# Optimization experiments

Hardware: AMD Instinct MI355X
Metric: run time of the kernel (lower is better)

The kernel has to match this reference:

```python
import jax, jax.numpy as jnp
import numpy as np

N, E, G, H, C, DIN, DE = 20000, 320000, 32, 8, 56, 32, 5
HC = H * C  # 448
NEG_SLOPE = 0.2
EPS_BN = 1e-5


def _seg_softmax(scores, seg, num):
    # scores: [E, H], softmax over edges sharing the same target node
    m = jax.ops.segment_max(scores, seg, num_segments=num)
    e = jnp.exp(scores - m[seg])
    s = jax.ops.segment_sum(e, seg, num_segments=num)
    return e / (s[seg] + 1e-16)


def _add_self_loops(src, dst, eattr, n):
    # PyG fill_value='mean': self-loop edge_attr = mean of incoming edge_attr
    deg = jax.ops.segment_sum(jnp.ones((src.shape[0],), eattr.dtype), dst, num_segments=n)
    esum = jax.ops.segment_sum(eattr, dst, num_segments=n)
    loop_attr = esum / jnp.maximum(deg, 1.0)[:, None]
    ar = jnp.arange(n, dtype=src.dtype)
    return (jnp.concatenate([src, ar]), jnp.concatenate([dst, ar]),
            jnp.concatenate([eattr, loop_attr], axis=0))


def _gatv2(x, src, dst, eattr, Wl, Wr, We, att, bias, n):
    xl = (x @ Wl).reshape(n, H, C)  # source transform (messages)
    xr = (x @ Wr).reshape(n, H, C)  # target transform
    ee = (eattr @ We).reshape(-1, H, C)
    s = jax.nn.leaky_relu(xl[src] + xr[dst] + ee, NEG_SLOPE)  # [E, H, C]
    score = jnp.einsum('ehc,hc->eh', s, att)
    alpha = _seg_softmax(score, dst, n)
    out = jax.ops.segment_sum(alpha[..., None] * xl[src], dst, num_segments=n)
    return out.reshape(n, HC) + bias


def _bn(x, gamma, beta):
    m = x.mean(axis=0)
    v = x.var(axis=0)  # biased variance, as torch BatchNorm1d (training)
    return (x - m) * jax.lax.rsqrt(v + EPS_BN) * gamma + beta


def setup_inputs() -> dict:
    key = jax.random.key(0)
    ks = jax.random.split(key, 18)
    sc = lambda k, shape: (jax.random.normal(k, shape, jnp.float32) * 0.05)
    return {
        'x': jax.random.normal(ks[0], (N, DIN), jnp.float32),
        'edge_index': jax.random.randint(ks[1], (2, E), 0, N),
        'edge_attr': jax.random.normal(ks[2], (E, DE), jnp.float32),
        'batch': jnp.sort(jax.random.randint(ks[3], (N,), 0, G)),
        'Wl1': sc(ks[4], (DIN, HC)), 'Wr1': sc(ks[5], (DIN, HC)),
        'We1': sc(ks[6], (DE, HC)), 'att1': sc(ks[7], (H, C)),
        'bias1': jnp.zeros((HC,), jnp.float32),
        'Wl2': sc(ks[8], (HC, HC)), 'Wr2': sc(ks[9], (HC, HC)),
        'We2': sc(ks[10], (DE, HC)), 'att2': sc(ks[11], (H, C)),
        'bias2': jnp.zeros((HC,), jnp.float32),
        'bn_gamma': jnp.ones((HC,), jnp.float32),
        'bn_beta': jnp.zeros((HC,), jnp.float32),
        'Wlin': sc(ks[12], (HC, 18)),
        'blin': jnp.zeros((18,), jnp.float32),
    }


def reference(x, edge_index, edge_attr, batch, Wl1, Wr1, We1, att1, bias1,
              Wl2, Wr2, We2, att2, bias2, bn_gamma, bn_beta, Wlin, blin):
    src, dst = edge_index[0], edge_index[1]
    src2, dst2, ea2 = _add_self_loops(src, dst, edge_attr, N)
    # dropout is identity in eval
    h = _gatv2(x, src2, dst2, ea2, Wl1, Wr1, We1, att1, bias1, N)
    h = jax.nn.elu(h)
    h = _bn(h, bn_gamma, bn_beta)
    h = _gatv2(h, src2, dst2, ea2, Wl2, Wr2, We2, att2, bias2, N)
    # global mean pool per graph
    cnt = jax.ops.segment_sum(jnp.ones((N,), h.dtype), batch, num_segments=G)
    pooled = jax.ops.segment_sum(h, batch, num_segments=G) / jnp.maximum(cnt, 1.0)[:, None]
    pooled = _bn(pooled, bn_gamma, bn_beta)
    logits = pooled @ Wlin + blin
    return jax.nn.log_softmax(logits, axis=1)
```

## Files before the change

kernel.cpp:

```cpp
#include <hip/hip_runtime.h>
#include <hip/hip_bf16.h>

#define NN   20000
#define EE   320000
#define EN   340000
#define HH   8
#define CC   56
#define HC   448
#define DEA  5
#define EAS  8
#define DINN 32
#define GG   32
#define NEG  0.2f

#define SS   896
#define MT   157
#define NT   7

typedef short bf16x8 __attribute__((ext_vector_type(8)));
typedef float f32x4  __attribute__((ext_vector_type(4)));
typedef float f32x8  __attribute__((ext_vector_type(8)));

static __device__ __forceinline__ unsigned short f2bf(float f) {
  unsigned int u = __float_as_uint(f);
  u += 0x7fffu + ((u >> 16) & 1u);
  return (unsigned short)(u >> 16);
}

static __device__ __forceinline__ f32x8 bf8_to_f32x8(uint4 u) {
  f32x8 o;
  o[0] = __uint_as_float(u.x << 16); o[1] = __uint_as_float(u.x & 0xffff0000u);
  o[2] = __uint_as_float(u.y << 16); o[3] = __uint_as_float(u.y & 0xffff0000u);
  o[4] = __uint_as_float(u.z << 16); o[5] = __uint_as_float(u.z & 0xffff0000u);
  o[6] = __uint_as_float(u.w << 16); o[7] = __uint_as_float(u.w & 0xffff0000u);
  return o;
}

static __device__ __forceinline__ float dpp8_sum(float x) {
  int v = __float_as_int(x);
  x += __int_as_float(__builtin_amdgcn_update_dpp(0, v, 0xB1, 0xF, 0xF, true));
  v = __float_as_int(x);
  x += __int_as_float(__builtin_amdgcn_update_dpp(0, v, 0x4E, 0xF, 0xF, true));
  v = __float_as_int(x);
  x += __int_as_float(__builtin_amdgcn_update_dpp(0, v, 0x141, 0xF, 0xF, true));
  return x;
}

__global__ void k_deg(const int* __restrict__ dst, int* deg) {
  int e = blockIdx.x * 256 + threadIdx.x;
  if (e < EE) atomicAdd(&deg[dst[e]], 1);
}

__global__ __launch_bounds__(1024) void k_scan(const int* __restrict__ deg, int* offs,
                                               int* cursor) {
  __shared__ int tot[1024];
  int t = threadIdx.x;
  int base = t * 20;
  int loc[20];
  int s = 0;
  #pragma unroll
  for (int i = 0; i < 20; i++) {
    int idx = base + i;
    int v = (idx < NN) ? deg[idx] + 1 : 0;
    loc[i] = s;
    s += v;
  }
  tot[t] = s;
  __syncthreads();
  for (int o = 1; o < 1024; o <<= 1) {
    int v = (t >= o) ? tot[t - o] : 0;
    __syncthreads();
    tot[t] += v;
    __syncthreads();
  }
  int basesum = (t == 0) ? 0 : tot[t - 1];
  #pragma unroll
  for (int i = 0; i < 20; i++) {
    int idx = base + i;
    if (idx < NN) { offs[idx] = basesum + loc[i]; cursor[idx] = basesum + loc[i]; }
  }
  if (t == 1023) offs[NN] = tot[1023];
}

#define XCN (NN * DINN)
#define W1N (SS * DINN)
#define W2N (SS * HC)
__global__ void k_scatter(const int* __restrict__ src, const int* __restrict__ dst,
                          const float* __restrict__ ea,
                          int* cursor, int* __restrict__ csr_src, float* __restrict__ csr_ea,
                          const float* __restrict__ x, unsigned short* __restrict__ xb,
                          const float* __restrict__ Wl1, const float* __restrict__ Wr1,
                          unsigned short* __restrict__ W1t,
                          const float* __restrict__ Wl2, const float* __restrict__ Wr2,
                          unsigned short* __restrict__ W2t) {
  int i = blockIdx.x * 256 + threadIdx.x;
  if (i < EE) {
    int d = dst[i], s = src[i];
    float a[DEA];
    #pragma unroll
    for (int j = 0; j < DEA; j++) a[j] = ea[(size_t)i * DEA + j];
    int pos = atomicAdd(&cursor[d], 1);
    csr_src[pos] = s;
    float* o = csr_ea + (size_t)pos * EAS;
    *(f32x4*)o       = (f32x4){a[0], a[1], a[2], a[3]};
    *(f32x4*)(o + 4) = (f32x4){a[4], 0.f, 0.f, 0.f};
    return;
  }
  i -= EE;
  if (i < XCN) { xb[i] = f2bf(x[i]); return; }
  i -= XCN;
  if (i < W1N) {
    int col = i / DINN, k = i - col * DINN;
    int cc = (col < HC) ? col : col - HC;
    const float* W = (col < HC) ? Wl1 : Wr1;
    W1t[i] = f2bf(W[(size_t)k * HC + cc]);
    return;
  }
  i -= W1N;
  if (i < W2N) {
    int col = i / HC, k = i - col * HC;
    int cc = (col < HC) ? col : col - HC;
    const float* W = (col < HC) ? Wl2 : Wr2;
    W2t[i] = f2bf(W[(size_t)k * HC + cc]);
  }
}

__global__ void k_aux(const int* __restrict__ offs,
                      int* __restrict__ csr_src, float* __restrict__ csr_ea) {
  int n = blockIdx.x * 256 + threadIdx.x;
  if (n >= NN) return;
  int e0 = offs[n], e1 = offs[n + 1] - 1;
  float a0 = 0.f, a1 = 0.f, a2 = 0.f, a3 = 0.f, a4 = 0.f;
  for (int e = e0; e < e1; e++) {
    const float* p = csr_ea + (size_t)e * EAS;
    a0 += p[0]; a1 += p[1]; a2 += p[2]; a3 += p[3]; a4 += p[4];
  }
  float inv = 1.f / fmaxf((float)(e1 - e0), 1.f);
  csr_src[e1] = n;
  float* o = csr_ea + (size_t)e1 * EAS;
  *(f32x4*)o       = (f32x4){a0 * inv, a1 * inv, a2 * inv, a3 * inv};
  *(f32x4*)(o + 4) = (f32x4){a4 * inv, 0.f, 0.f, 0.f};
}

__global__ __launch_bounds__(256) void k_gemm1(const unsigned short* __restrict__ xb,
                                               const unsigned short* __restrict__ W1t,
                                               unsigned short* __restrict__ out) {
  int w = threadIdx.x >> 6, lane = threadIdx.x & 63;
  int q = lane >> 4, r = lane & 15;
  int m0 = blockIdx.x * 64;
  int node = blockIdx.y * 64 + w * 16 + r;
  int nc = node < NN ? node : NN - 1;
  bf16x8 b = *(const bf16x8*)(xb + (size_t)nc * DINN + q * 8);
  #pragma unroll
  for (int j = 0; j < 4; j++) {
    bf16x8 a = *(const bf16x8*)(W1t + (size_t)(m0 + j * 16 + r) * DINN + q * 8);
    f32x4 acc = {0.f, 0.f, 0.f, 0.f};
    acc = __builtin_amdgcn_mfma_f32_16x16x32_bf16(a, b, acc, 0, 0, 0);
    uint2 st;
    st.x = ((unsigned int)f2bf(acc[1]) << 16) | f2bf(acc[0]);
    st.y = ((unsigned int)f2bf(acc[3]) << 16) | f2bf(acc[2]);
    if (node < NN)
      *(uint2*)(out + (size_t)node * SS + m0 + j * 16 + q * 4) = st;
  }
}

__global__ __launch_bounds__(256) void k_attn(
    const unsigned short* __restrict__ xlr,
    const int* __restrict__ offs, const int* __restrict__ csr_src,
    const float* __restrict__ csr_ea,
    const float* __restrict__ We, const float* __restrict__ att,
    const float* __restrict__ bias,
    unsigned short* __restrict__ outb, int layer1) {
  int n = __builtin_amdgcn_readfirstlane(blockIdx.x * 4 + (threadIdx.x >> 6));
  if (n >= NN) return;
  int lane = threadIdx.x & 63;
  int head = lane >> 3, sub = lane & 7;
  bool v = sub < 7;
  int cb = head * 56 + (v ? sub : 6) * 8;

  f32x8 z = {0.f,0.f,0.f,0.f,0.f,0.f,0.f,0.f};
  f32x8 xr = bf8_to_f32x8(*(const uint4*)(xlr + (size_t)n * SS + HC + cb));
  f32x8 at = *(const f32x8*)(att + cb);
  if (!v) at = z;
  f32x8 w0 = *(const f32x8*)(We + 0 * HC + cb);
  f32x8 w1 = *(const f32x8*)(We + 1 * HC + cb);
  f32x8 w2 = *(const f32x8*)(We + 2 * HC + cb);
  f32x8 w3 = *(const f32x8*)(We + 3 * HC + cb);
  f32x8 w4 = *(const f32x8*)(We + 4 * HC + cb);

  int e0 = offs[n], e1 = offs[n + 1];
  int last = e1 - 1;
  float l = 0.f;
  f32x8 acc = z;

  int sA[4];
  #pragma unroll
  for (int k = 0; k < 4; k++) {
    int ek = e0 + k; ek = ek < last ? ek : last;
    sA[k] = csr_src[__builtin_amdgcn_readfirstlane(ek)];
  }

  for (int e = e0; e < e1; e += 4) {
    uint4 g[4];
    #pragma unroll
    for (int k = 0; k < 4; k++)
      g[k] = *(const uint4*)(xlr + (size_t)sA[k] * SS + cb);
    int en = e + 4;
    if (en < e1) {
      #pragma unroll
      for (int k = 0; k < 4; k++) {
        int ek = en + k; ek = ek < last ? ek : last;
        sA[k] = csr_src[__builtin_amdgcn_readfirstlane(ek)];
      }
    }
    f32x8 md[4];
    #pragma unroll
    for (int k = 0; k < 4; k++) {
      int ek = e + k; ek = ek < last ? ek : last;
      md[k] = *(const f32x8*)(csr_ea + (size_t)__builtin_amdgcn_readfirstlane(ek) * EAS);
    }

    #pragma unroll
    for (int k = 0; k < 4; k++) {
      f32x8 tb = xr;
      tb += md[k][0] * w0; tb += md[k][1] * w1; tb += md[k][2] * w2;
      tb += md[k][3] * w3; tb += md[k][4] * w4;
      f32x8 xl = bf8_to_f32x8(g[k]);
      f32x8 t = tb + xl;
      #pragma unroll
      for (int i = 0; i < 8; i++) t[i] = fmaxf(t[i], NEG * t[i]);
      float p = 0.f;
      #pragma unroll
      for (int i = 0; i < 8; i++) p += t[i] * at[i];
      p = dpp8_sum(p);
      float wv = (e + k < e1) ? __expf(fminf(p, 60.f)) : 0.f;
      acc += wv * xl;
      l += wv;
    }
  }

  f32x8 b8 = *(const f32x8*)(bias + cb);
  f32x8 o = acc * (1.f / (l + 1e-16f)) + b8;
  if (v) {
    if (layer1) {
      #pragma unroll
      for (int i = 0; i < 8; i++) o[i] = o[i] > 0.f ? o[i] : (__expf(o[i]) - 1.f);
    }
    uint4 pk;
    pk.x = ((unsigned int)f2bf(o[1]) << 16) | f2bf(o[0]);
    pk.y = ((unsigned int)f2bf(o[3]) << 16) | f2bf(o[2]);
    pk.z = ((unsigned int)f2bf(o[5]) << 16) | f2bf(o[4]);
    pk.w = ((unsigned int)f2bf(o[7]) << 16) | f2bf(o[6]);
    *(uint4*)(outb + (size_t)n * HC + cb) = pk;
  }
}

__global__ __launch_bounds__(448) void k_bnstats(const unsigned short* __restrict__ h,
                                                 float* stat) {
  int c = threadIdx.x;
  int rows_per = (NN + gridDim.x - 1) / gridDim.x;
  int r0 = blockIdx.x * rows_per, r1 = min(NN, r0 + rows_per);
  float s = 0.f, sq = 0.f;
  for (int r = r0; r < r1; r++) {
    unsigned int u = h[(size_t)r * HC + c];
    float v = __uint_as_float(u << 16);
    s += v; sq += v * v;
  }
  atomicAdd(&stat[c], s);
  atomicAdd(&stat[HC + c], sq);
}

__global__ __launch_bounds__(64) void k_w2fix(const unsigned short* __restrict__ W2t,
                                              const float* __restrict__ stat,
                                              const float* __restrict__ gam,
                                              const float* __restrict__ bet,
                                              unsigned short* __restrict__ W2s,
                                              float* __restrict__ bias2) {
  int j = blockIdx.x;
  int t = threadIdx.x;
  float bacc = 0.f;
  #pragma unroll
  for (int it = 0; it < 7; it++) {
    int k = t + it * 64;
    float w = __uint_as_float((unsigned int)W2t[(size_t)j * HC + k] << 16);
    float mean = stat[k] * (1.f / NN);
    float var  = stat[HC + k] * (1.f / NN) - mean * mean;
    float sc = rsqrtf(var + 1e-5f) * gam[k];
    float sh = bet[k] - mean * sc;
    bacc += sh * w;
    W2s[(size_t)j * HC + k] = f2bf(sc * w);
  }
  #pragma unroll
  for (int m = 32; m >= 1; m >>= 1) bacc += __shfl_xor(bacc, m, 64);
  if (t == 0) bias2[j] = bacc;
}

__global__ __launch_bounds__(256) void k_gemm2(const unsigned short* __restrict__ A,
                                               const unsigned short* __restrict__ Bt,
                                               const float* __restrict__ bias2,
                                               unsigned short* __restrict__ out) {
  __shared__ unsigned short As[2 * 128 * 64];
  __shared__ unsigned short Bs[2 * 128 * 64];
  int bid = blockIdx.x;
  int g = bid / 56, rem = bid - g * 56;
  int xs = min(8, MT - g * 8);
  int bx = g * 8 + rem % xs;
  int by = rem / xs;
  int t = threadIdx.x;
  int w = t >> 6, lane = t & 63;
  int wm = w >> 1, wn = w & 1;
  int q = lane >> 4, r = lane & 15;
  int m0 = bx * 128;
  int n0 = by * 128;

  const unsigned short *ag[4], *bg[4];
  unsigned short *la[4], *lb[4];
  #pragma unroll
  for (int j = 0; j < 4; j++) {
    int s = t + j * 256;
    int row = s >> 3;
    int gcol = (s & 7) ^ (row & 7);
    int ar = m0 + row; if (ar >= NN) ar = NN - 1;
    ag[j] = A + (size_t)ar * HC + gcol * 8;
    bg[j] = Bt + (size_t)(n0 + row) * HC + gcol * 8;
    la[j] = As + s * 8;
    lb[j] = Bs + s * 8;
  }

  f32x4 zero = {0.f, 0.f, 0.f, 0.f};
  f32x4 acc[4][4];
  #pragma unroll
  for (int i = 0; i < 4; i++)
    #pragma unroll
    for (int j = 0; j < 4; j++) acc[i][j] = zero;

#define G2_STAGE(buf, k0)                                                     \
  _Pragma("unroll")                                                           \
  for (int j = 0; j < 4; j++) {                                               \
    __builtin_amdgcn_global_load_lds(                                         \
        (const __attribute__((address_space(1))) unsigned int*)(ag[j] + (k0)),\
        (__attribute__((address_space(3))) unsigned int*)(la[j] + (buf) * (128 * 64)), \
        16, 0, 0);                                                            \
    __builtin_amdgcn_global_load_lds(                                         \
        (const __attribute__((address_space(1))) unsigned int*)(bg[j] + (k0)),\
        (__attribute__((address_space(3))) unsigned int*)(lb[j] + (buf) * (128 * 64)), \
        16, 0, 0);                                                            \
  }

  G2_STAGE(0, 0);
  for (int st = 0; st < NT; ++st) {
    int cur = st & 1;
    if (st < NT - 1) {
      G2_STAGE(cur ^ 1, (st + 1) * 64);
      asm volatile("s_waitcnt vmcnt(8)" ::: "memory");
    } else {
      asm volatile("s_waitcnt vmcnt(0)" ::: "memory");
    }
    __builtin_amdgcn_s_barrier();
    const unsigned short* Asc = As + cur * (128 * 64);
    const unsigned short* Bsc = Bs + cur * (128 * 64);
    #pragma unroll
    for (int kk = 0; kk < 64; kk += 32) {
      int p = (kk >> 3) + q;
      bf16x8 af[4], bf[4];
      #pragma unroll
      for (int i = 0; i < 4; i++) {
        int row = wm * 64 + i * 16 + r;
        af[i] = *(const bf16x8*)(Asc + row * 64 + ((p ^ (r & 7)) * 8));
      }
      #pragma unroll
      for (int j = 0; j < 4; j++) {
        int row = wn * 64 + j * 16 + r;
        bf[j] = *(const bf16x8*)(Bsc + row * 64 + ((p ^ (r & 7)) * 8));
      }
      #pragma unroll
      for (int i = 0; i < 4; i++)
        #pragma unroll
        for (int j = 0; j < 4; j++)
          acc[i][j] = __builtin_amdgcn_mfma_f32_16x16x32_bf16(af[i], bf[j], acc[i][j], 0, 0, 0);
    }
    __builtin_amdgcn_s_barrier();
  }
#undef G2_STAGE

  #pragma unroll
  for (int j = 0; j < 4; j++) {
    int col = n0 + wn * 64 + j * 16 + r;
    float bs = bias2[col];
    #pragma unroll
    for (int i = 0; i < 4; i++) {
      int row_base = m0 + wm * 64 + i * 16 + q * 4;
      #pragma unroll
      for (int reg = 0; reg < 4; reg++) {
        int row = row_base + reg;
        if (row < NN) out[(size_t)row * SS + col] = f2bf(acc[i][j][reg] + bs);
      }
    }
  }
}

__global__ __launch_bounds__(448) void k_pool(const unsigned short* __restrict__ h2,
                                              const int* __restrict__ batch,
                                              float* pooled, int* cnt) {
  int c = threadIdx.x;
  int rows_per = (NN + gridDim.x - 1) / gridDim.x;
  int r0 = blockIdx.x * rows_per, r1 = min(NN, r0 + rows_per);
  if (r0 >= r1) return;
  float loc = 0.f;
  int rc = 0;
  int gcur = batch[r0];
  for (int r = r0; r < r1; r++) {
    int g = batch[r];
    if (g != gcur) {
      atomicAdd(&pooled[gcur * HC + c], loc);
      if (c == 0) atomicAdd(&cnt[gcur], rc);
      loc = 0.f; rc = 0; gcur = g;
    }
    unsigned int u = h2[(size_t)r * HC + c];
    loc += __uint_as_float(u << 16);
    rc++;
  }
  atomicAdd(&pooled[gcur * HC + c], loc);
  if (c == 0) atomicAdd(&cnt[gcur], rc);
}

__global__ __launch_bounds__(448) void k_final(const float* __restrict__ pooled_sum,
                                               const int* __restrict__ cnt,
                                               const float* __restrict__ gam,
                                               const float* __restrict__ bet,
                                               const float* __restrict__ Wlin,
                                               const float* __restrict__ blin,
                                               float* __restrict__ out) {
  __shared__ float P[GG * HC];
  __shared__ float L[GG * 18];
  __shared__ float red[GG];
  int c = threadIdx.x;
  float s = 0.f, sq = 0.f;
  for (int g = 0; g < GG; g++) {
    float v = pooled_sum[g * HC + c] / fmaxf((float)cnt[g], 1.f);
    P[g * HC + c] = v; s += v; sq += v * v;
  }
  float mean = s * (1.f / GG);
  float var  = sq * (1.f / GG) - mean * mean;
  float sc = rsqrtf(var + 1e-5f) * gam[c];
  float sh = bet[c] - mean * sc;
  for (int g = 0; g < GG; g++) P[g * HC + c] = P[g * HC + c] * sc + sh;
  __syncthreads();
  for (int o = c; o < GG * 18; o += HC) {
    int g = o / 18, j = o - g * 18;
    float acc = blin[j];
    for (int k = 0; k < HC; k++) acc += P[g * HC + k] * Wlin[k * 18 + j];
    L[o] = acc;
  }
  __syncthreads();
  if (c < GG) {
    float mx = -3.4e38f;
    for (int j = 0; j < 18; j++) mx = fmaxf(mx, L[c * 18 + j]);
    float se = 0.f;
    for (int j = 0; j < 18; j++) se += __expf(L[c * 18 + j] - mx);
    red[c] = mx + logf(se);
  }
  __syncthreads();
  for (int o = c; o < GG * 18; o += HC) out[o] = L[o] - red[o / 18];
}

extern "C" void kernel_launch(void* const* d_in, const int* in_sizes, int n_in,
                              void* d_out, int out_size, void* d_ws, size_t ws_size,
                              hipStream_t stream) {
  (void)in_sizes; (void)n_in; (void)out_size; (void)ws_size;
  const float* x     = (const float*)d_in[0];
  const int*   ei    = (const int*)d_in[1];
  const float* ea    = (const float*)d_in[2];
  const int*   batch = (const int*)d_in[3];
  const float* Wl1   = (const float*)d_in[4];
  const float* Wr1   = (const float*)d_in[5];
  const float* We1   = (const float*)d_in[6];
  const float* att1  = (const float*)d_in[7];
  const float* bias1 = (const float*)d_in[8];
  const float* Wl2   = (const float*)d_in[9];
  const float* Wr2   = (const float*)d_in[10];
  const float* We2   = (const float*)d_in[11];
  const float* att2  = (const float*)d_in[12];
  const float* bias2in = (const float*)d_in[13];
  const float* gam   = (const float*)d_in[14];
  const float* bet   = (const float*)d_in[15];
  const float* Wlin  = (const float*)d_in[16];
  const float* blin  = (const float*)d_in[17];
  float* out = (float*)d_out;
  const int* srcp = ei;
  const int* dstp = ei + EE;

  char* ws = (char*)d_ws;
  size_t off = 0;
  auto alloc = [&](size_t bytes) -> char* {
    char* p = ws + off;
    off = (off + bytes + 255) & ~(size_t)255;
    return p;
  };
  int*   deg     = (int*)  alloc(NN * 4);
  float* bnstat  = (float*)alloc(HC * 2 * 4);
  float* pooled  = (float*)alloc(GG * HC * 4 + GG * 4);
  int*   cnt     = (int*)(pooled + GG * HC);
  size_t zlen    = (size_t)((char*)(cnt + GG) - (char*)deg);

  int*   offs    = (int*)  alloc((NN + 1) * 4);
  int*   cursor  = (int*)  alloc(NN * 4);
  int*   csr_src = (int*)  alloc((size_t)EN * 4);
  float* csr_ea  = (float*)alloc((size_t)EN * EAS * 4);
  unsigned short* xlr = (unsigned short*)alloc((size_t)NN * SS * 2);
  unsigned short* h1b = (unsigned short*)alloc((size_t)NN * HC * 2);
  unsigned short* h2b = (unsigned short*)alloc((size_t)NN * HC * 2);
  unsigned short* xb  = (unsigned short*)alloc((size_t)NN * DINN * 2);
  unsigned short* W1t = (unsigned short*)alloc((size_t)SS * DINN * 2);
  unsigned short* W2t = (unsigned short*)alloc((size_t)SS * HC * 2);
  unsigned short* W2s = (unsigned short*)alloc((size_t)SS * HC * 2);
  float* bias2   = (float*)alloc(SS * 4);

  hipMemsetAsync(deg, 0, zlen, stream);
  k_deg<<<(EE + 255) / 256, 256, 0, stream>>>(dstp, deg);
  k_scan<<<1, 1024, 0, stream>>>(deg, offs, cursor);
  k_scatter<<<(EE + XCN + W1N + W2N + 255) / 256, 256, 0, stream>>>(
      srcp, dstp, ea, cursor, csr_src, csr_ea, x, xb, Wl1, Wr1, W1t, Wl2, Wr2, W2t);
  k_aux<<<(NN + 255) / 256, 256, 0, stream>>>(offs, csr_src, csr_ea);

  dim3 g1(SS / 64, (NN + 63) / 64);
  k_gemm1<<<g1, 256, 0, stream>>>(xb, W1t, xlr);
  k_attn<<<(NN + 3) / 4, 256, 0, stream>>>(xlr, offs, csr_src, csr_ea,
                                           We1, att1, bias1, h1b, 1);
  k_bnstats<<<512, HC, 0, stream>>>(h1b, bnstat);
  k_w2fix<<<SS, 64, 0, stream>>>(W2t, bnstat, gam, bet, W2s, bias2);

  k_gemm2<<<MT * NT, 256, 0, stream>>>(h1b, W2s, bias2, xlr);
  k_attn<<<(NN + 3) / 4, 256, 0, stream>>>(xlr, offs, csr_src, csr_ea,
                                           We2, att2, bias2in, h2b, 0);

  k_pool<<<640, HC, 0, stream>>>(h2b, batch, pooled, cnt);
  k_final<<<1, HC, 0, stream>>>(pooled, cnt, gam, bet, Wlin, blin, out);
}
```

Measured before the change: 431.6 us.

## Merge preprocessing kernels and compute self-loop edge attributes inside layer-1 attention

The degree count is folded into the conversion kernel, and the CSR scatter shares one launch with the first GEMM. The scan now writes the self-loop source indices. The separate self-loop mean kernel is removed: layer-1 attention sums incoming edge attributes while streaming them, then handles the self-loop edge itself and writes the mean attribute for layer 2. This removes two launches and one pass over the edge attributes, but the layer-1 attention kernel now writes to csr_ea and carries a padding correction that adds small complexity.

After: 433.6 us. About the same (+0.5%).

```diff
diff --git a/kernel.cpp b/kernel.cpp
--- a/kernel.cpp
+++ b/kernel.cpp
@@ -17,6 +17,10 @@
 #define MT   157
 #define NT   7
 
+#define SCB  1250
+#define G1X  14
+#define G1Y  313
+
 typedef short bf16x8 __attribute__((ext_vector_type(8)));
 typedef float f32x4  __attribute__((ext_vector_type(4)));
 typedef float f32x8  __attribute__((ext_vector_type(8)));
@@ -46,66 +50,17 @@
   return x;
 }
 
-__global__ void k_deg(const int* __restrict__ dst, int* deg) {
-  int e = blockIdx.x * 256 + threadIdx.x;
-  if (e < EE) atomicAdd(&deg[dst[e]], 1);
-}
-
-__global__ __launch_bounds__(1024) void k_scan(const int* __restrict__ deg, int* offs,
-                                               int* cursor) {
-  __shared__ int tot[1024];
-  int t = threadIdx.x;
-  int base = t * 20;
-  int loc[20];
-  int s = 0;
-  #pragma unroll
-  for (int i = 0; i < 20; i++) {
-    int idx = base + i;
-    int v = (idx < NN) ? deg[idx] + 1 : 0;
-    loc[i] = s;
-    s += v;
-  }
-  tot[t] = s;
-  __syncthreads();
-  for (int o = 1; o < 1024; o <<= 1) {
-    int v = (t >= o) ? tot[t - o] : 0;
-    __syncthreads();
-    tot[t] += v;
-    __syncthreads();
-  }
-  int basesum = (t == 0) ? 0 : tot[t - 1];
-  #pragma unroll
-  for (int i = 0; i < 20; i++) {
-    int idx = base + i;
-    if (idx < NN) { offs[idx] = basesum + loc[i]; cursor[idx] = basesum + loc[i]; }
-  }
-  if (t == 1023) offs[NN] = tot[1023];
-}
-
 #define XCN (NN * DINN)
 #define W1N (SS * DINN)
 #define W2N (SS * HC)
-__global__ void k_scatter(const int* __restrict__ src, const int* __restrict__ dst,
-                          const float* __restrict__ ea,
-                          int* cursor, int* __restrict__ csr_src, float* __restrict__ csr_ea,
-                          const float* __restrict__ x, unsigned short* __restrict__ xb,
-                          const float* __restrict__ Wl1, const float* __restrict__ Wr1,
-                          unsigned short* __restrict__ W1t,
-                          const float* __restrict__ Wl2, const float* __restrict__ Wr2,
-                          unsigned short* __restrict__ W2t) {
+__global__ void k_pre(const int* __restrict__ dst, int* deg,
+                      const float* __restrict__ x, unsigned short* __restrict__ xb,
+                      const float* __restrict__ Wl1, const float* __restrict__ Wr1,
+                      unsigned short* __restrict__ W1t,
+                      const float* __restrict__ Wl2, const float* __restrict__ Wr2,
+                      unsigned short* __restrict__ W2t) {
   int i = blockIdx.x * 256 + threadIdx.x;
-  if (i < EE) {
-    int d = dst[i], s = src[i];
-    float a[DEA];
-    #pragma unroll
-    for (int j = 0; j < DEA; j++) a[j] = ea[(size_t)i * DEA + j];
-    int pos = atomicAdd(&cursor[d], 1);
-    csr_src[pos] = s;
-    float* o = csr_ea + (size_t)pos * EAS;
-    *(f32x4*)o       = (f32x4){a[0], a[1], a[2], a[3]};
-    *(f32x4*)(o + 4) = (f32x4){a[4], 0.f, 0.f, 0.f};
-    return;
-  }
+  if (i < EE) { atomicAdd(&deg[dst[i]], 1); return; }
   i -= EE;
   if (i < XCN) { xb[i] = f2bf(x[i]); return; }
   i -= XCN;
@@ -125,30 +80,68 @@
   }
 }
 
-__global__ void k_aux(const int* __restrict__ offs,
-                      int* __restrict__ csr_src, float* __restrict__ csr_ea) {
-  int n = blockIdx.x * 256 + threadIdx.x;
-  if (n >= NN) return;
-  int e0 = offs[n], e1 = offs[n + 1] - 1;
-  float a0 = 0.f, a1 = 0.f, a2 = 0.f, a3 = 0.f, a4 = 0.f;
-  for (int e = e0; e < e1; e++) {
-    const float* p = csr_ea + (size_t)e * EAS;
-    a0 += p[0]; a1 += p[1]; a2 += p[2]; a3 += p[3]; a4 += p[4];
-  }
-  float inv = 1.f / fmaxf((float)(e1 - e0), 1.f);
-  csr_src[e1] = n;
-  float* o = csr_ea + (size_t)e1 * EAS;
-  *(f32x4*)o       = (f32x4){a0 * inv, a1 * inv, a2 * inv, a3 * inv};
-  *(f32x4*)(o + 4) = (f32x4){a4 * inv, 0.f, 0.f, 0.f};
-}
-
-__global__ __launch_bounds__(256) void k_gemm1(const unsigned short* __restrict__ xb,
-                                               const unsigned short* __restrict__ W1t,
-                                               unsigned short* __restrict__ out) {
+__global__ __launch_bounds__(1024) void k_scan(const int* __restrict__ deg, int* offs,
+                                               int* cursor, int* __restrict__ csr_src) {
+  __shared__ int tot[1024];
+  int t = threadIdx.x;
+  int base = t * 20;
+  int loc[20];
+  int s = 0;
+  #pragma unroll
+  for (int i = 0; i < 20; i++) {
+    int idx = base + i;
+    int v = (idx < NN) ? deg[idx] + 1 : 0;
+    loc[i] = s;
+    s += v;
+  }
+  tot[t] = s;
+  __syncthreads();
+  for (int o = 1; o < 1024; o <<= 1) {
+    int v = (t >= o) ? tot[t - o] : 0;
+    __syncthreads();
+    tot[t] += v;
+    __syncthreads();
+  }
+  int basesum = (t == 0) ? 0 : tot[t - 1];
+  #pragma unroll
+  for (int i = 0; i < 20; i++) {
+    int idx = base + i;
+    if (idx < NN) {
+      int o0 = basesum + loc[i];
+      offs[idx] = o0; cursor[idx] = o0;
+      int slot = (i < 19) ? (basesum + loc[i + 1] - 1) : (tot[t] - 1);
+      csr_src[slot] = idx;
+    }
+  }
+  if (t == 1023) offs[NN] = tot[1023];
+}
+
+__global__ __launch_bounds__(256) void k_scg(
+    const int* __restrict__ src, const int* __restrict__ dst,
+    const float* __restrict__ ea, int* cursor,
+    int* __restrict__ csr_src, float* __restrict__ csr_ea,
+    const unsigned short* __restrict__ xb, const unsigned short* __restrict__ W1t,
+    unsigned short* __restrict__ xlr) {
+  if (blockIdx.x < SCB) {
+    int i = blockIdx.x * 256 + threadIdx.x;
+    if (i >= EE) return;
+    int d = dst[i], s = src[i];
+    float a[DEA];
+    #pragma unroll
+    for (int j = 0; j < DEA; j++) a[j] = ea[(size_t)i * DEA + j];
+    int pos = atomicAdd(&cursor[d], 1);
+    csr_src[pos] = s;
+    float* o = csr_ea + (size_t)pos * EAS;
+    *(f32x4*)o       = (f32x4){a[0], a[1], a[2], a[3]};
+    *(f32x4*)(o + 4) = (f32x4){a[4], 0.f, 0.f, 0.f};
+    return;
+  }
+  int gid = blockIdx.x - SCB;
+  int bx = gid % G1X, by = gid / G1X;
   int w = threadIdx.x >> 6, lane = threadIdx.x & 63;
   int q = lane >> 4, r = lane & 15;
-  int m0 = blockIdx.x * 64;
-  int node = blockIdx.y * 64 + w * 16 + r;
+  int m0 = bx * 64;
+  int node = by * 64 + w * 16 + r;
   int nc = node < NN ? node : NN - 1;
   bf16x8 b = *(const bf16x8*)(xb + (size_t)nc * DINN + q * 8);
   #pragma unroll
@@ -160,17 +153,18 @@
     st.x = ((unsigned int)f2bf(acc[1]) << 16) | f2bf(acc[0]);
     st.y = ((unsigned int)f2bf(acc[3]) << 16) | f2bf(acc[2]);
     if (node < NN)
-      *(uint2*)(out + (size_t)node * SS + m0 + j * 16 + q * 4) = st;
-  }
-}
-
+      *(uint2*)(xlr + (size_t)node * SS + m0 + j * 16 + q * 4) = st;
+  }
+}
+
+template <int L1>
 __global__ __launch_bounds__(256) void k_attn(
     const unsigned short* __restrict__ xlr,
     const int* __restrict__ offs, const int* __restrict__ csr_src,
-    const float* __restrict__ csr_ea,
+    float* __restrict__ csr_ea,
     const float* __restrict__ We, const float* __restrict__ att,
     const float* __restrict__ bias,
-    unsigned short* __restrict__ outb, int layer1) {
+    unsigned short* __restrict__ outb) {
   int n = __builtin_amdgcn_readfirstlane(blockIdx.x * 4 + (threadIdx.x >> 6));
   if (n >= NN) return;
   int lane = threadIdx.x & 63;
@@ -190,34 +184,44 @@
 
   int e0 = offs[n], e1 = offs[n + 1];
   int last = e1 - 1;
+  int er1 = L1 ? last : e1;
+  int lc = er1 - 1; if (lc < e0) lc = e0;
   float l = 0.f;
   f32x8 acc = z;
+  float ua0 = 0.f, ua1 = 0.f, ua2 = 0.f, ua3 = 0.f, ua4 = 0.f;
 
   int sA[4];
   #pragma unroll
   for (int k = 0; k < 4; k++) {
-    int ek = e0 + k; ek = ek < last ? ek : last;
+    int ek = e0 + k; ek = ek < lc ? ek : lc;
     sA[k] = csr_src[__builtin_amdgcn_readfirstlane(ek)];
   }
 
-  for (int e = e0; e < e1; e += 4) {
+  for (int e = e0; e < er1; e += 4) {
     uint4 g[4];
     #pragma unroll
     for (int k = 0; k < 4; k++)
       g[k] = *(const uint4*)(xlr + (size_t)sA[k] * SS + cb);
     int en = e + 4;
-    if (en < e1) {
+    if (en < er1) {
       #pragma unroll
       for (int k = 0; k < 4; k++) {
-        int ek = en + k; ek = ek < last ? ek : last;
+        int ek = en + k; ek = ek < lc ? ek : lc;
         sA[k] = csr_src[__builtin_amdgcn_readfirstlane(ek)];
       }
     }
     f32x8 md[4];
     #pragma unroll
     for (int k = 0; k < 4; k++) {
-      int ek = e + k; ek = ek < last ? ek : last;
+      int ek = e + k; ek = ek < lc ? ek : lc;
       md[k] = *(const f32x8*)(csr_ea + (size_t)__builtin_amdgcn_readfirstlane(ek) * EAS);
+    }
+    if (L1) {
+      #pragma unroll
+      for (int k = 0; k < 4; k++) {
+        ua0 += md[k][0]; ua1 += md[k][1]; ua2 += md[k][2];
+        ua3 += md[k][3]; ua4 += md[k][4];
+      }
     }
 
     #pragma unroll
@@ -233,16 +237,47 @@
       #pragma unroll
       for (int i = 0; i < 8; i++) p += t[i] * at[i];
       p = dpp8_sum(p);
-      float wv = (e + k < e1) ? __expf(fminf(p, 60.f)) : 0.f;
+      float wv = (e + k < er1) ? __expf(fminf(p, 60.f)) : 0.f;
       acc += wv * xl;
       l += wv;
     }
+  }
+
+  if (L1) {
+    int deg = er1 - e0;
+    if (deg > 0) {
+      int padded = ((deg + 3) >> 2) << 2;
+      float extra = (float)(padded - deg);
+      f32x8 ml = *(const f32x8*)(csr_ea + (size_t)__builtin_amdgcn_readfirstlane(lc) * EAS);
+      ua0 -= extra * ml[0]; ua1 -= extra * ml[1]; ua2 -= extra * ml[2];
+      ua3 -= extra * ml[3]; ua4 -= extra * ml[4];
+    }
+    float inv = 1.f / fmaxf((float)deg, 1.f);
+    float m0 = ua0 * inv, m1 = ua1 * inv, m2 = ua2 * inv,
+          m3 = ua3 * inv, m4 = ua4 * inv;
+    if (lane == 0) {
+      float* o = csr_ea + (size_t)last * EAS;
+      *(f32x4*)o       = (f32x4){m0, m1, m2, m3};
+      *(f32x4*)(o + 4) = (f32x4){m4, 0.f, 0.f, 0.f};
+    }
+    f32x8 xls = bf8_to_f32x8(*(const uint4*)(xlr + (size_t)n * SS + cb));
+    f32x8 t = xr + xls;
+    t += m0 * w0; t += m1 * w1; t += m2 * w2; t += m3 * w3; t += m4 * w4;
+    #pragma unroll
+    for (int i = 0; i < 8; i++) t[i] = fmaxf(t[i], NEG * t[i]);
+    float p = 0.f;
+    #pragma unroll
+    for (int i = 0; i < 8; i++) p += t[i] * at[i];
+    p = dpp8_sum(p);
+    float wv = __expf(fminf(p, 60.f));
+    acc += wv * xls;
+    l += wv;
   }
 
   f32x8 b8 = *(const f32x8*)(bias + cb);
   f32x8 o = acc * (1.f / (l + 1e-16f)) + b8;
   if (v) {
-    if (layer1) {
+    if (L1) {
       #pragma unroll
       for (int i = 0; i < 8; i++) o[i] = o[i] > 0.f ? o[i] : (__expf(o[i]) - 1.f);
     }
@@ -517,22 +552,20 @@
   float* bias2   = (float*)alloc(SS * 4);
 
   hipMemsetAsync(deg, 0, zlen, stream);
-  k_deg<<<(EE + 255) / 256, 256, 0, stream>>>(dstp, deg);
-  k_scan<<<1, 1024, 0, stream>>>(deg, offs, cursor);
-  k_scatter<<<(EE + XCN + W1N + W2N + 255) / 256, 256, 0, stream>>>(
-      srcp, dstp, ea, cursor, csr_src, csr_ea, x, xb, Wl1, Wr1, W1t, Wl2, Wr2, W2t);
-  k_aux<<<(NN + 255) / 256, 256, 0, stream>>>(offs, csr_src, csr_ea);
-
-  dim3 g1(SS / 64, (NN + 63) / 64);
-  k_gemm1<<<g1, 256, 0, stream>>>(xb, W1t, xlr);
-  k_attn<<<(NN + 3) / 4, 256, 0, stream>>>(xlr, offs, csr_src, csr_ea,
-                                           We1, att1, bias1, h1b, 1);
+  k_pre<<<(EE + XCN + W1N + W2N + 255) / 256, 256, 0, stream>>>(
+      dstp, deg, x, xb, Wl1, Wr1, W1t, Wl2, Wr2, W2t);
+  k_scan<<<1, 1024, 0, stream>>>(deg, offs, cursor, csr_src);
+  k_scg<<<SCB + G1X * G1Y, 256, 0, stream>>>(
+      srcp, dstp, ea, cursor, csr_src, csr_ea, xb, W1t, xlr);
+
+  k_attn<1><<<(NN + 3) / 4, 256, 0, stream>>>(xlr, offs, csr_src, csr_ea,
+                                              We1, att1, bias1, h1b);
   k_bnstats<<<512, HC, 0, stream>>>(h1b, bnstat);
   k_w2fix<<<SS, 64, 0, stream>>>(W2t, bnstat, gam, bet, W2s, bias2);
 
   k_gemm2<<<MT * NT, 256, 0, stream>>>(h1b, W2s, bias2, xlr);
-  k_attn<<<(NN + 3) / 4, 256, 0, stream>>>(xlr, offs, csr_src, csr_ea,
-                                           We2, att2, bias2in, h2b, 0);
+  k_attn<0><<<(NN + 3) / 4, 256, 0, stream>>>(xlr, offs, csr_src, csr_ea,
+                                              We2, att2, bias2in, h2b);
 
   k_pool<<<640, HC, 0, stream>>>(h2b, batch, pooled, cnt);
   k_final<<<1, HC, 0, stream>>>(pooled, cnt, gam, bet, Wlin, blin, out);
```
